# Performance work log

Hardware: AMD Instinct MI355X
Metric: run time of the kernel (lower is better)

## Reference

```python
import jax, jax.numpy as jnp
import numpy as np

B, T, C, H = 8, 2048, 1024, 1024
SCALE = 1.0 / np.sqrt(H).astype(np.float32)


def setup_inputs() -> dict:
    key = jax.random.key(0)
    kx, kq, kk, kv = jax.random.split(key, 4)
    x = jax.random.normal(kx, (B, T, C), dtype=jnp.float32)
    # Linear(C -> H, bias=False): store weights as [C, H] so y = x @ W
    Wq = jax.random.normal(kq, (C, H), dtype=jnp.float32) * (1.0 / np.sqrt(C))
    Wk = jax.random.normal(kk, (C, H), dtype=jnp.float32) * (1.0 / np.sqrt(C))
    Wv = jax.random.normal(kv, (C, H), dtype=jnp.float32) * (1.0 / np.sqrt(C))
    return {"x": x, "Wq": Wq, "Wk": Wk, "Wv": Wv}


def reference(x, Wq, Wk, Wv):
    # Projections
    Q = jnp.einsum('btc,ch->bth', x, Wq)
    K = jnp.einsum('btc,ch->bth', x, Wk)
    V = jnp.einsum('btc,ch->bth', x, Wv)
    t = x.shape[1]
    # Scaled dot-product scores with causal mask
    attn = jnp.einsum('bqh,bkh->bqk', Q, K) * SCALE  # [B,T,T]
    causal = jnp.tril(jnp.ones((t, t), dtype=bool))
    attn = jnp.where(causal, attn, -jnp.inf)
    scores = jax.nn.softmax(attn, axis=-1)
    # dropout p=0.0 (eval/deterministic) -> identity
    out = jnp.einsum('bqk,bkh->bqh', scores, V)
    return out
```

## Files before the change

kernel.cpp:

```cpp
#include <hip/hip_runtime.h>


#define BM 128
#define BN 128
#define BK 32

typedef __attribute__((ext_vector_type(8))) __bf16 bf16x8;
typedef __attribute__((ext_vector_type(4))) float floatx4;

__device__ __forceinline__ unsigned short f2bf(float f) {
  unsigned int u = __float_as_uint(f);
  u += 0x7fffu + ((u >> 16) & 1u);
  return (unsigned short)(u >> 16);
}
__device__ __forceinline__ float bf2f(unsigned short s) {
  return __uint_as_float(((unsigned int)s) << 16);
}

__device__ __forceinline__ void gload_lds16(const unsigned short* g, unsigned short* l) {
  __builtin_amdgcn_global_load_lds(
      (const __attribute__((address_space(1))) void*)g,
      (__attribute__((address_space(3))) void*)l,
      16, 0, 0);
}

__device__ __forceinline__ void gemm_mainloop(
    const unsigned short* __restrict__ A, int lda,
    const unsigned short* __restrict__ Bt, int ldb,
    int m0, int n0, int kTiles,
    unsigned short* As, unsigned short* Bs,
    floatx4 (&acc)[4][4])
{
  const int tid  = threadIdx.x;
  const int wave = tid >> 6;
  const int lane = tid & 63;
  const int wr = wave >> 1;
  const int wc = wave & 1;

  const int c0 = wave * 2;
  const int c1 = c0 + 1;
  const int r0 = c0 * 16 + (lane >> 2);
  const int r1 = c1 * 16 + (lane >> 2);
  const int ck = (lane & 3) * 8;

  const unsigned short* pA0 = A  + (size_t)(m0 + r0) * lda + ck;
  const unsigned short* pA1 = A  + (size_t)(m0 + r1) * lda + ck;
  const unsigned short* pB0 = Bt + (size_t)(n0 + r0) * ldb + ck;
  const unsigned short* pB1 = Bt + (size_t)(n0 + r1) * ldb + ck;

  unsigned short* lA0 = As + c0 * 512;
  unsigned short* lA1 = As + c1 * 512;
  unsigned short* lB0 = Bs + c0 * 512;
  unsigned short* lB1 = Bs + c1 * 512;

  const int fr = lane & 15;
  const int kq = (lane >> 4) * 8;

  for (int kt = 0; kt < kTiles; ++kt) {
    __syncthreads();
    gload_lds16(pA0, lA0);
    gload_lds16(pA1, lA1);
    gload_lds16(pB0, lB0);
    gload_lds16(pB1, lB1);
    pA0 += BK; pA1 += BK; pB0 += BK; pB1 += BK;
    __syncthreads();

    bf16x8 af[4], bg[4];
#pragma unroll
    for (int i = 0; i < 4; ++i)
      af[i] = *(const bf16x8*)(As + ((wr * 64 + i * 16 + fr) * BK + kq));
#pragma unroll
    for (int j = 0; j < 4; ++j)
      bg[j] = *(const bf16x8*)(Bs + ((wc * 64 + j * 16 + fr) * BK + kq));
#pragma unroll
    for (int i = 0; i < 4; ++i)
#pragma unroll
      for (int j = 0; j < 4; ++j)
        acc[i][j] = __builtin_amdgcn_mfma_f32_16x16x32_bf16(af[i], bg[j], acc[i][j], 0, 0, 0);
  }
}

#define ACC_INIT(acc)                         \
  do {                                        \
    floatx4 z_ = {0.f, 0.f, 0.f, 0.f};        \
    _Pragma("unroll")                         \
    for (int i_ = 0; i_ < 4; ++i_)            \
      _Pragma("unroll")                       \
      for (int j_ = 0; j_ < 4; ++j_)          \
        acc[i_][j_] = z_;                     \
  } while (0)


__global__ void cvt_x_kernel(const float* __restrict__ x, unsigned short* __restrict__ xb) {
  int idx = (blockIdx.x * 256 + threadIdx.x) * 4;
  float4 v = *(const float4*)(x + idx);
  ushort4 o;
  o.x = f2bf(v.x); o.y = f2bf(v.y); o.z = f2bf(v.z); o.w = f2bf(v.w);
  *(ushort4*)(xb + idx) = o;
}

__global__ void cvt_w_kernel(const float* __restrict__ W, unsigned short* __restrict__ Wt) {
  __shared__ unsigned short tile[64][65];
  const int k0 = blockIdx.x * 64, n0 = blockIdx.y * 64;
  const int tid = threadIdx.x, tx = tid & 63, ty = tid >> 6;
#pragma unroll
  for (int r = 0; r < 64; r += 4)
    tile[r + ty][tx] = f2bf(W[(size_t)(k0 + r + ty) * 1024 + (n0 + tx)]);
  __syncthreads();
#pragma unroll
  for (int r = 0; r < 64; r += 4)
    Wt[(size_t)(n0 + r + ty) * 1024 + (k0 + tx)] = tile[tx][r + ty];
}

__global__ void zero_l_kernel(float* __restrict__ l) {
  l[blockIdx.x * 256 + threadIdx.x] = 0.f;
}

__global__ __launch_bounds__(256) void gemm_qkv_kernel(
    const unsigned short* __restrict__ xb,
    const unsigned short* __restrict__ Wt,
    unsigned short* __restrict__ Q,
    unsigned short* __restrict__ K,
    unsigned short* __restrict__ V)
{
  __shared__ __align__(16) unsigned short As[BM * BK];
  __shared__ __align__(16) unsigned short Bs[BN * BK];
  floatx4 acc[4][4];
  ACC_INIT(acc);
  const int m0 = blockIdx.x * BM;
  const int n0 = blockIdx.y * BN;
  gemm_mainloop(xb, 1024, Wt, 1024, m0, n0, 1024 / BK, As, Bs, acc);

  unsigned short* const dsts[3] = {Q, K, V};
  unsigned short* D = dsts[n0 >> 10];
  const int ncol0 = n0 & 1023;

  const int tid = threadIdx.x, wave = tid >> 6, lane = tid & 63;
  const int wr = wave >> 1, wc = wave & 1;
  const int rb = m0 + wr * 64 + ((lane >> 4) << 2);
  const int cb = ncol0 + wc * 64 + (lane & 15);
#pragma unroll
  for (int i = 0; i < 4; ++i)
#pragma unroll
    for (int j = 0; j < 4; ++j)
#pragma unroll
      for (int r = 0; r < 4; ++r)
        D[(size_t)(rb + i * 16 + r) * 1024 + (cb + j * 16)] = f2bf(acc[i][j][r]);
}

__global__ void transpose_v_kernel(const unsigned short* __restrict__ V,
                                   unsigned short* __restrict__ Vt) {
  __shared__ unsigned short tile[64][68];
  const int b = blockIdx.z;
  const int t0 = blockIdx.x * 64, h0 = blockIdx.y * 64;
  const int tid = threadIdx.x;
  const int cx = (tid & 15) * 4;
  const int ry = tid >> 4;
  const unsigned short* Vb = V + (size_t)b * 2048 * 1024;
#pragma unroll
  for (int r = 0; r < 64; r += 16) {
    ushort4 v = *(const ushort4*)(Vb + (size_t)(t0 + r + ry) * 1024 + (h0 + cx));
    *(ushort4*)&tile[r + ry][cx] = v;
  }
  __syncthreads();
  unsigned short* Vtb = Vt + (size_t)b * 1024 * 2048;
#pragma unroll
  for (int r = 0; r < 64; r += 16) {
    const int h = r + ry;
    ushort4 o;
    o.x = tile[cx][h]; o.y = tile[cx + 1][h]; o.z = tile[cx + 2][h]; o.w = tile[cx + 3][h];
    *(ushort4*)(Vtb + (size_t)(h0 + h) * 2048 + (t0 + cx)) = o;
  }
}

__global__ __launch_bounds__(256) void gemm_scores_kernel(
    const unsigned short* __restrict__ Q,
    const unsigned short* __restrict__ K,
    unsigned short* __restrict__ S,
    float* __restrict__ lsum)
{
  const int b = blockIdx.x & 7;
  const int t = blockIdx.x >> 3;
  int mi = (int)((sqrtf(8.f * (float)t + 1.f) - 1.f) * 0.5f);
  while ((mi + 1) * (mi + 2) / 2 <= t) ++mi;
  while (mi * (mi + 1) / 2 > t) --mi;
  const int ni = t - mi * (mi + 1) / 2;
  const int m0 = mi * BM;
  const int n0 = ni * BN;

  __shared__ __align__(16) unsigned short As[BM * BK];
  __shared__ __align__(16) unsigned short Bs[BN * BK];
  floatx4 acc[4][4];
  ACC_INIT(acc);
  const unsigned short* Qb = Q + (size_t)b * 2048 * 1024;
  const unsigned short* Kb = K + (size_t)b * 2048 * 1024;
  gemm_mainloop(Qb, 1024, Kb, 1024, m0, n0, 1024 / BK, As, Bs, acc);

  unsigned short* Sb = S + (size_t)b * 2048 * 2048;
  float* lb = lsum + b * 2048;
  const int tid = threadIdx.x, wave = tid >> 6, lane = tid & 63;
  const int wr = wave >> 1, wc = wave & 1;
  const int rb = m0 + wr * 64 + ((lane >> 4) << 2);
  const int cb = n0 + wc * 64 + (lane & 15);

  float rsum[4][4];
#pragma unroll
  for (int i = 0; i < 4; ++i)
#pragma unroll
    for (int r = 0; r < 4; ++r)
      rsum[i][r] = 0.f;

#pragma unroll
  for (int i = 0; i < 4; ++i)
#pragma unroll
    for (int j = 0; j < 4; ++j)
#pragma unroll
      for (int r = 0; r < 4; ++r) {
        const int tq = rb + i * 16 + r;
        const int tk = cb + j * 16;
        float e = 0.f;
        if (tk <= tq) e = __expf(acc[i][j][r] * 0.03125f);
        const unsigned short h = f2bf(e);
        Sb[(size_t)tq * 2048 + tk] = h;
        rsum[i][r] += bf2f(h);
      }

#pragma unroll
  for (int off = 1; off < 16; off <<= 1)
#pragma unroll
    for (int i = 0; i < 4; ++i)
#pragma unroll
      for (int r = 0; r < 4; ++r)
        rsum[i][r] += __shfl_xor(rsum[i][r], off, 64);

  if ((lane & 15) == 0) {
#pragma unroll
    for (int i = 0; i < 4; ++i)
#pragma unroll
      for (int r = 0; r < 4; ++r)
        atomicAdd(&lb[rb + i * 16 + r], rsum[i][r]);
  }
}

__global__ __launch_bounds__(256) void gemm_pv_kernel(
    const unsigned short* __restrict__ S,
    const unsigned short* __restrict__ Vt,
    const float* __restrict__ lsum,
    float* __restrict__ out)
{
  const int b = blockIdx.x & 7;
  const int r2 = blockIdx.x >> 3;
  const int mi = 15 - (r2 >> 3);
  const int ni = r2 & 7;
  const int m0 = mi * BM;
  const int n0 = ni * BN;

  __shared__ __align__(16) unsigned short As[BM * BK];
  __shared__ __align__(16) unsigned short Bs[BN * BK];
  floatx4 acc[4][4];
  ACC_INIT(acc);
  const unsigned short* Pb = S  + (size_t)b * 2048 * 2048;
  const unsigned short* Vb = Vt + (size_t)b * 1024 * 2048;
  const int kTiles = m0 / BK + BM / BK;
  gemm_mainloop(Pb, 2048, Vb, 2048, m0, n0, kTiles, As, Bs, acc);

  float* Ob = out + (size_t)b * 2048 * 1024;
  const float* lb = lsum + b * 2048;
  const int tid = threadIdx.x, wave = tid >> 6, lane = tid & 63;
  const int wr = wave >> 1, wc = wave & 1;
  const int rb = m0 + wr * 64 + ((lane >> 4) << 2);
  const int cb = n0 + wc * 64 + (lane & 15);

  float inv[4][4];
#pragma unroll
  for (int i = 0; i < 4; ++i)
#pragma unroll
    for (int r = 0; r < 4; ++r)
      inv[i][r] = 1.0f / lb[rb + i * 16 + r];

#pragma unroll
  for (int i = 0; i < 4; ++i)
#pragma unroll
    for (int j = 0; j < 4; ++j)
#pragma unroll
      for (int r = 0; r < 4; ++r)
        Ob[(size_t)(rb + i * 16 + r) * 1024 + (cb + j * 16)] = acc[i][j][r] * inv[i][r];
}


extern "C" void kernel_launch(void* const* d_in, const int* in_sizes, int n_in,
                              void* d_out, int out_size, void* d_ws, size_t ws_size,
                              hipStream_t stream) {
  const float* x  = (const float*)d_in[0];
  const float* Wq = (const float*)d_in[1];
  const float* Wk = (const float*)d_in[2];
  const float* Wv = (const float*)d_in[3];
  float* out = (float*)d_out;

  char* ws = (char*)d_ws;
  unsigned short* xb  = (unsigned short*)(ws);
  unsigned short* Wt  = (unsigned short*)(ws + 33554432ull);
  unsigned short* Q   = (unsigned short*)(ws + 39845888ull);
  unsigned short* K   = (unsigned short*)(ws + 73400320ull);
  unsigned short* V   = (unsigned short*)(ws + 106954752ull);
  unsigned short* Vt  = (unsigned short*)(ws + 140509184ull);
  unsigned short* S   = (unsigned short*)(ws + 174063616ull);
  float*          l   = (float*)ws;

  cvt_x_kernel<<<16384, 256, 0, stream>>>(x, xb);
  dim3 gw(16, 16);
  cvt_w_kernel<<<gw, 256, 0, stream>>>(Wq, Wt);
  cvt_w_kernel<<<gw, 256, 0, stream>>>(Wk, Wt + 1024 * 1024);
  cvt_w_kernel<<<gw, 256, 0, stream>>>(Wv, Wt + 2 * 1024 * 1024);

  gemm_qkv_kernel<<<dim3(128, 24), 256, 0, stream>>>(xb, Wt, Q, K, V);

  transpose_v_kernel<<<dim3(32, 16, 8), 256, 0, stream>>>(V, Vt);
  zero_l_kernel<<<64, 256, 0, stream>>>(l);
  gemm_scores_kernel<<<8 * 136, 256, 0, stream>>>(Q, K, S, l);
  gemm_pv_kernel<<<1024, 256, 0, stream>>>(S, Vt, l, out);
}
```

Measured before the change: 395.7 us.

## Rewrite QKV GEMM with 256x256 tiles, triple-buffered LDS and XCD-aware block mapping

The QKV projection GEMM moves from a 128x128 tile with 4 waves to a 256x256 tile with 8 waves. It uses a dedicated 3-stage LDS pipeline built on direct global-to-LDS loads with XOR swizzling, vmcnt-based waits and s_setprio around the MFMA block. Block indices are remapped so that consecutive blocks on each XCD share A/B panels, improving L2 reuse. The larger tiles raise arithmetic intensity, but each thread holds more accumulator registers and the grid has fewer blocks (768).

```diff
diff --git a/kernel.cpp b/kernel.cpp
--- a/kernel.cpp
+++ b/kernel.cpp
@@ -23,6 +23,7 @@
       (__attribute__((address_space(3))) void*)l,
       16, 0, 0);
 }
+
 
 __device__ __forceinline__ void gemm_mainloop(
     const unsigned short* __restrict__ A, int lda,
@@ -116,31 +117,113 @@
   l[blockIdx.x * 256 + threadIdx.x] = 0.f;
 }
 
-__global__ __launch_bounds__(256) void gemm_qkv_kernel(
+__global__ __launch_bounds__(512, 2) void gemm_qkv_kernel(
     const unsigned short* __restrict__ xb,
     const unsigned short* __restrict__ Wt,
     unsigned short* __restrict__ Q,
     unsigned short* __restrict__ K,
     unsigned short* __restrict__ V)
 {
-  __shared__ __align__(16) unsigned short As[BM * BK];
-  __shared__ __align__(16) unsigned short Bs[BN * BK];
-  floatx4 acc[4][4];
-  ACC_INIT(acc);
-  const int m0 = blockIdx.x * BM;
-  const int n0 = blockIdx.y * BN;
-  gemm_mainloop(xb, 1024, Wt, 1024, m0, n0, 1024 / BK, As, Bs, acc);
+  __shared__ __align__(16) unsigned short lds[49152];
+
+  const int bid = blockIdx.x;
+  const int lin = (bid & 7) * 96 + (bid >> 3);
+  const int ni = lin >> 6;
+  const int mi = lin & 63;
+  const int m0 = mi * 256;
+  const int n0 = ni * 256;
+
+  const int tid = threadIdx.x;
+  const int w = tid >> 6;
+  const int l = tid & 63;
+  const int wr = w >> 2;
+  const int wc = w & 3;
+
+  const int sr0 = w * 16 + (l >> 2);
+  const int sr1 = 128 + sr0;
+  const int sc  = l & 3;
+  const int scs = ((sc ^ (sr0 & 3)) << 3);
+
+  const unsigned short* pA0 = xb + (size_t)(m0 + sr0) * 1024 + scs;
+  const unsigned short* pA1 = xb + (size_t)(m0 + sr1) * 1024 + scs;
+  const unsigned short* pB0 = Wt + (size_t)(n0 + sr0) * 1024 + scs;
+  const unsigned short* pB1 = Wt + (size_t)(n0 + sr1) * 1024 + scs;
+
+  const int stgW = w * 512;
+
+#define QKV_STAGE(slot)                                          \
+  do {                                                           \
+    unsigned short* _sA = &lds[(slot) * 8192 + stgW];            \
+    unsigned short* _sB = &lds[24576 + (slot) * 8192 + stgW];    \
+    gload_lds16(pA0, _sA);                                       \
+    gload_lds16(pA1, _sA + 4096);                                \
+    gload_lds16(pB0, _sB);                                       \
+    gload_lds16(pB1, _sB + 4096);                                \
+    pA0 += 32; pA1 += 32; pB0 += 32; pB1 += 32;                  \
+  } while (0)
+
+  const int fr = l & 15;
+  const int q  = l >> 4;
+  const int cks = (q ^ (fr & 3)) * 8;
+  const int aOff = (wr * 128 + fr) * 32 + cks;
+  const int bOff = (wc * 64 + fr) * 32 + cks;
+
+  floatx4 acc[8][4];
+  {
+    floatx4 z = {0.f, 0.f, 0.f, 0.f};
+#pragma unroll
+    for (int i = 0; i < 8; ++i)
+#pragma unroll
+      for (int j = 0; j < 4; ++j)
+        acc[i][j] = z;
+  }
+
+  QKV_STAGE(0);
+  QKV_STAGE(1);
+  asm volatile("s_waitcnt vmcnt(4)" ::: "memory");
+  __builtin_amdgcn_s_barrier();
+
+  int curSlot = 0, swSlot = 2;
+  for (int kt = 0; kt < 32; ++kt) {
+    const unsigned short* sA = &lds[curSlot * 8192];
+    const unsigned short* sB = &lds[24576 + curSlot * 8192];
+
+    bf16x8 a[8], b[4];
+#pragma unroll
+    for (int i = 0; i < 8; ++i)
+      a[i] = *(const bf16x8*)(sA + aOff + i * 512);
+#pragma unroll
+    for (int j = 0; j < 4; ++j)
+      b[j] = *(const bf16x8*)(sB + bOff + j * 512);
+
+    if (kt < 30) QKV_STAGE(swSlot);
+
+    __builtin_amdgcn_s_setprio(1);
+#pragma unroll
+    for (int i = 0; i < 8; ++i)
+#pragma unroll
+      for (int j = 0; j < 4; ++j)
+        acc[i][j] = __builtin_amdgcn_mfma_f32_16x16x32_bf16(a[i], b[j], acc[i][j], 0, 0, 0);
+    __builtin_amdgcn_s_setprio(0);
+
+    if (kt < 31) {
+      if (kt < 30) asm volatile("s_waitcnt vmcnt(4)" ::: "memory");
+      else         asm volatile("s_waitcnt vmcnt(0)" ::: "memory");
+      __builtin_amdgcn_s_barrier();
+    }
+    curSlot = (curSlot == 2) ? 0 : curSlot + 1;
+    swSlot  = (swSlot  == 2) ? 0 : swSlot  + 1;
+  }
+#undef QKV_STAGE
 
   unsigned short* const dsts[3] = {Q, K, V};
   unsigned short* D = dsts[n0 >> 10];
   const int ncol0 = n0 & 1023;
 
-  const int tid = threadIdx.x, wave = tid >> 6, lane = tid & 63;
-  const int wr = wave >> 1, wc = wave & 1;
-  const int rb = m0 + wr * 64 + ((lane >> 4) << 2);
-  const int cb = ncol0 + wc * 64 + (lane & 15);
-#pragma unroll
-  for (int i = 0; i < 4; ++i)
+  const int rb = m0 + wr * 128 + (q << 2);
+  const int cb = ncol0 + wc * 64 + fr;
+#pragma unroll
+  for (int i = 0; i < 8; ++i)
 #pragma unroll
     for (int j = 0; j < 4; ++j)
 #pragma unroll
@@ -313,7 +396,7 @@
   cvt_w_kernel<<<gw, 256, 0, stream>>>(Wk, Wt + 1024 * 1024);
   cvt_w_kernel<<<gw, 256, 0, stream>>>(Wv, Wt + 2 * 1024 * 1024);
 
-  gemm_qkv_kernel<<<dim3(128, 24), 256, 0, stream>>>(xb, Wt, Q, K, V);
+  gemm_qkv_kernel<<<768, 512, 0, stream>>>(xb, Wt, Q, K, V);
 
   transpose_v_kernel<<<dim3(32, 16, 8), 256, 0, stream>>>(V, Vt);
   zero_l_kernel<<<64, 256, 0, stream>>>(l);
```

Result: faster. 379.2 us (-4.2%).

## Rewrite QKV projection GEMM as 256x256 tile, 8-wave, double-buffered pipelined kernel

Applied to the files above, without the earlier changes.

Replaces the 128x128 QKV GEMM with a 256x256 output tile per 512-thread block. It streams 64-wide K slices into a 128KB LDS region with XOR-swizzled direct global-to-LDS loads, and interleaves the loads with MFMA phases using explicit barriers, waitcnt and setprio. Block IDs are remapped so that neighbouring M tiles land on the same XCD for L2 reuse. The intent is to raise arithmetic intensity and hide memory latency in the largest projection GEMM, at the cost of heavy register/LDS use and fragile hand-scheduled synchronisation.

```diff
diff --git a/kernel.cpp b/kernel.cpp
--- a/kernel.cpp
+++ b/kernel.cpp
@@ -23,6 +23,7 @@
       (__attribute__((address_space(3))) void*)l,
       16, 0, 0);
 }
+
 
 __device__ __forceinline__ void gemm_mainloop(
     const unsigned short* __restrict__ A, int lda,
@@ -116,36 +117,181 @@
   l[blockIdx.x * 256 + threadIdx.x] = 0.f;
 }
 
-__global__ __launch_bounds__(256) void gemm_qkv_kernel(
+__global__ __launch_bounds__(512, 2) void gemm_qkv_kernel(
     const unsigned short* __restrict__ xb,
     const unsigned short* __restrict__ Wt,
     unsigned short* __restrict__ Q,
     unsigned short* __restrict__ K,
     unsigned short* __restrict__ V)
 {
-  __shared__ __align__(16) unsigned short As[BM * BK];
-  __shared__ __align__(16) unsigned short Bs[BN * BK];
-  floatx4 acc[4][4];
-  ACC_INIT(acc);
-  const int m0 = blockIdx.x * BM;
-  const int n0 = blockIdx.y * BN;
-  gemm_mainloop(xb, 1024, Wt, 1024, m0, n0, 1024 / BK, As, Bs, acc);
+  __shared__ __align__(16) unsigned short lds[65536];
+
+  const int bid = blockIdx.x;
+  const int xcd = bid & 7;
+  const int local = bid >> 3;
+  const int mi = xcd * 8 + (local & 7);
+  const int ni = local >> 3;
+  const int m0 = mi * 256;
+  const int n0 = ni * 256;
+
+  const int tid = threadIdx.x;
+  const int w = tid >> 6;
+  const int l = tid & 63;
+  const int wr = w >> 2;
+  const int wc = w & 3;
+
+  const int srcRow = w * 8 + (l >> 3);
+  const int chunkSrc = (((l & 7) ^ ((l >> 3) & 7)) << 3);
+  const unsigned short* pAs = xb + (size_t)(m0 + srcRow) * 1024 + chunkSrc;
+  const unsigned short* pBs = Wt + (size_t)(n0 + srcRow) * 1024 + chunkSrc;
+  const int stgW = w * 512;
+
+#define STG(gbase, ldsOff)                                      \
+  do {                                                          \
+    gload_lds16((gbase), &lds[(ldsOff) + stgW]);                \
+    gload_lds16((gbase) + 65536, &lds[(ldsOff) + stgW + 4096]); \
+  } while (0)
+
+  const int fr = l & 15;
+  const int kq = l >> 4;
+  const int ac0 = ((kq)     ^ (fr & 7)) << 3;
+  const int ac1 = ((4 + kq) ^ (fr & 7)) << 3;
+  const int aBase = wr * 8192 + fr * 64;
+  const int bBase = 16384 + (wc >> 1) * 8192 + ((wc & 1) * 64 + fr) * 64;
+
+#define RD_A(BUF, MH)                                                          \
+  do {                                                                         \
+    _Pragma("unroll")                                                          \
+    for (int f = 0; f < 4; ++f) {                                              \
+      a[2*f]   = *(const bf16x8*)(lds + (BUF) + aBase + ((MH)*4+f)*1024 + ac0);\
+      a[2*f+1] = *(const bf16x8*)(lds + (BUF) + aBase + ((MH)*4+f)*1024 + ac1);\
+    }                                                                          \
+  } while (0)
+#define RD_B(BUF, NH)                                                          \
+  do {                                                                         \
+    _Pragma("unroll")                                                          \
+    for (int n = 0; n < 2; ++n) {                                              \
+      b[2*((NH)*2+n)]   = *(const bf16x8*)(lds + (BUF) + bBase + ((NH)*2+n)*1024 + ac0); \
+      b[2*((NH)*2+n)+1] = *(const bf16x8*)(lds + (BUF) + bBase + ((NH)*2+n)*1024 + ac1); \
+    }                                                                          \
+  } while (0)
+
+#define PH_OPEN()                                             \
+  do {                                                        \
+    __builtin_amdgcn_s_barrier();                             \
+    asm volatile("s_waitcnt lgkmcnt(0)" ::: "memory");        \
+    __builtin_amdgcn_sched_barrier(0);                        \
+  } while (0)
+
+#define PH_MFMA(MB, NB)                                                        \
+  do {                                                                         \
+    __builtin_amdgcn_s_setprio(1);                                             \
+    _Pragma("unroll")                                                          \
+    for (int f = 0; f < 4; ++f)                                                \
+      _Pragma("unroll")                                                        \
+      for (int n = 0; n < 2; ++n) {                                            \
+        acc[(MB)+f][(NB)+n] = __builtin_amdgcn_mfma_f32_16x16x32_bf16(         \
+            a[2*f],   b[2*((NB)+n)],   acc[(MB)+f][(NB)+n], 0, 0, 0);          \
+        acc[(MB)+f][(NB)+n] = __builtin_amdgcn_mfma_f32_16x16x32_bf16(         \
+            a[2*f+1], b[2*((NB)+n)+1], acc[(MB)+f][(NB)+n], 0, 0, 0);          \
+      }                                                                        \
+    __builtin_amdgcn_s_setprio(0);                                             \
+  } while (0)
+
+  floatx4 acc[8][4];
+  {
+    floatx4 z = {0.f, 0.f, 0.f, 0.f};
+#pragma unroll
+    for (int i = 0; i < 8; ++i)
+#pragma unroll
+      for (int j = 0; j < 4; ++j)
+        acc[i][j] = z;
+  }
+  bf16x8 a[8], b[8];
+
+  STG(pAs,            0);
+  STG(pAs + 131072,   8192);
+  STG(pBs,            16384);
+  STG(pBs + 131072,   24576);
+  STG(pBs + 64,           49152);
+  STG(pBs + 64 + 131072,  57344);
+  asm volatile("s_waitcnt vmcnt(4)" ::: "memory");
+  __builtin_amdgcn_s_barrier();
+
+#pragma unroll 1
+  for (int j = 0; j < 8; ++j) {
+    const bool st2 = (j < 7);
+
+    RD_A(0, 0); RD_B(0, 0);
+    STG(pAs + 64, 32768);
+    PH_OPEN();
+    PH_MFMA(0, 0);
+    __builtin_amdgcn_s_barrier();
+
+    RD_B(0, 1);
+    STG(pAs + 64 + 131072, 40960);
+    PH_OPEN();
+    PH_MFMA(0, 2);
+    __builtin_amdgcn_s_barrier();
+
+    RD_A(0, 1);
+    if (st2) STG(pBs + 128, 16384);
+    PH_OPEN();
+    PH_MFMA(4, 0);
+    __builtin_amdgcn_s_barrier();
+
+    if (st2) STG(pBs + 128 + 131072, 24576);
+    PH_OPEN();
+    PH_MFMA(4, 2);
+    if (st2) asm volatile("s_waitcnt vmcnt(4)" ::: "memory");
+    else     asm volatile("s_waitcnt vmcnt(0)" ::: "memory");
+    __builtin_amdgcn_s_barrier();
+
+    RD_A(32768, 0); RD_B(32768, 0);
+    if (st2) STG(pAs + 128, 0);
+    PH_OPEN();
+    PH_MFMA(0, 0);
+    __builtin_amdgcn_s_barrier();
+
+    RD_B(32768, 1);
+    if (st2) STG(pAs + 128 + 131072, 8192);
+    PH_OPEN();
+    PH_MFMA(0, 2);
+    __builtin_amdgcn_s_barrier();
+
+    RD_A(32768, 1);
+    if (st2) STG(pBs + 192, 49152);
+    PH_OPEN();
+    PH_MFMA(4, 0);
+    __builtin_amdgcn_s_barrier();
+
+    if (st2) STG(pBs + 192 + 131072, 57344);
+    PH_OPEN();
+    PH_MFMA(4, 2);
+    if (st2) asm volatile("s_waitcnt vmcnt(4)" ::: "memory");
+    __builtin_amdgcn_s_barrier();
+
+    pAs += 128; pBs += 128;
+  }
+#undef STG
+#undef RD_A
+#undef RD_B
+#undef PH_OPEN
+#undef PH_MFMA
 
   unsigned short* const dsts[3] = {Q, K, V};
   unsigned short* D = dsts[n0 >> 10];
   const int ncol0 = n0 & 1023;
 
-  const int tid = threadIdx.x, wave = tid >> 6, lane = tid & 63;
-  const int wr = wave >> 1, wc = wave & 1;
-  const int rb = m0 + wr * 64 + ((lane >> 4) << 2);
-  const int cb = ncol0 + wc * 64 + (lane & 15);
-#pragma unroll
-  for (int i = 0; i < 4; ++i)
-#pragma unroll
-    for (int j = 0; j < 4; ++j)
+  const int rb = m0 + wr * 128 + (kq << 2);
+  const int cb = ncol0 + wc * 64 + fr;
+#pragma unroll
+  for (int i = 0; i < 8; ++i)
+#pragma unroll
+    for (int jj = 0; jj < 4; ++jj)
 #pragma unroll
       for (int r = 0; r < 4; ++r)
-        D[(size_t)(rb + i * 16 + r) * 1024 + (cb + j * 16)] = f2bf(acc[i][j][r]);
+        D[(size_t)(rb + i * 16 + r) * 1024 + (cb + jj * 16)] = f2bf(acc[i][jj][r]);
 }
 
 __global__ void transpose_v_kernel(const unsigned short* __restrict__ V,
@@ -313,7 +459,7 @@
   cvt_w_kernel<<<gw, 256, 0, stream>>>(Wk, Wt + 1024 * 1024);
   cvt_w_kernel<<<gw, 256, 0, stream>>>(Wv, Wt + 2 * 1024 * 1024);
 
-  gemm_qkv_kernel<<<dim3(128, 24), 256, 0, stream>>>(xb, Wt, Q, K, V);
+  gemm_qkv_kernel<<<768, 512, 0, stream>>>(xb, Wt, Q, K, V);
 
   transpose_v_kernel<<<dim3(32, 16, 8), 256, 0, stream>>>(V, Vt);
   zero_l_kernel<<<64, 256, 0, stream>>>(l);
```

New measurement: 365.8 us. 7.6% less time.
